# Optimization experiments

Hardware: AMD Instinct MI355X
Metric: run time of the kernel (lower is better)

Reference implementation:

```python
import jax, jax.numpy as jnp
import numpy as np


def _conv(x, w, b=None, stride=1, pad=1, groups=1):
    y = jax.lax.conv_general_dilated(
        x, w, (stride, stride), [(pad, pad), (pad, pad)],
        dimension_numbers=('NCHW', 'OIHW', 'NCHW'), feature_group_count=groups)
    return y if b is None else y + b[None, :, None, None]


def _dwt(x):
    # Haar DWT as grouped stride-2 conv, filters pre-flipped as in the torch code
    ll = np.array([[0.5, 0.5], [0.5, 0.5]])
    lh = np.array([[-0.5, -0.5], [0.5, 0.5]])
    hl = np.array([[-0.5, 0.5], [-0.5, 0.5]])
    hh = np.array([[0.5, -0.5], [-0.5, 0.5]])
    filts = np.stack([f[None, ::-1, ::-1] for f in (ll, lh, hl, hh)], 0)  # [4,1,2,2]
    w = jnp.asarray(np.concatenate([filts] * 3, 0), x.dtype)  # [12,1,2,2], groups=3
    return _conv(x, w, None, stride=2, pad=0, groups=3)


def setup_inputs():
    key = jax.random.key(0)
    ks = iter(jax.random.split(key, 64))
    def w(*shape):
        return jax.random.normal(next(ks), shape, jnp.float32) * 0.05
    B, H, W = 4, 512, 512
    F = 32  # number_f
    d = {'x': jax.random.uniform(next(ks), (B, 3, H, W), jnp.float32)}
    d['enc1_w'] = w(F, 3, 3, 3); d['enc1_b'] = w(F)
    for i in range(2, 6):
        d['enc%d_w' % i] = w(F, F, 3, 3); d['enc%d_b' % i] = w(F)
    d['cdc_w'] = w(F, F, 3, 3)                      # central-difference conv, no bias
    d['ct_w'] = w(64, 9, 3, 3); d['ct_b'] = w(64)   # conv_theta on 9-ch high_freq
    d['t1_w'] = w(64, 64, 1, 1); d['t1_b'] = w(64)
    d['t2_w'] = w(64, 64, 1, 1); d['t2_b'] = w(64)
    d['t3_w'] = w(1, 64, 1, 1); d['t3_b'] = w(1)
    d['lf_w'] = w(64, 3, 3, 3); d['lf_b'] = w(64)   # low_freq conv on haar_A
    d['fc1_w'] = w(512, 64); d['fc1_b'] = w(512)
    d['fc2_w'] = w(512, 512); d['fc2_b'] = w(512)
    d['fc3_w'] = w(512, 512); d['fc3_b'] = w(512)
    d['g_w'] = w(F, 512); d['g_b'] = w(F)           # to_gamma_0
    d['be_w'] = w(F, 512); d['be_b'] = w(F)         # to_beta_0
    d['res_w'] = w(F, F, 3, 3); d['res_b'] = w(F)
    d['d1_w'] = w(F, F, 3, 3); d['d1_b'] = w(F)
    d['d2_w'] = w(1, F, 3, 3); d['d2_b'] = w(1)
    return d


def reference(x, enc1_w, enc1_b, enc2_w, enc2_b, enc3_w, enc3_b, enc4_w, enc4_b,
              enc5_w, enc5_b, cdc_w, ct_w, ct_b, t1_w, t1_b, t2_w, t2_b, t3_w, t3_b,
              lf_w, lf_b, fc1_w, fc1_b, fc2_w, fc2_b, fc3_w, fc3_b,
              g_w, g_b, be_w, be_b, res_w, res_b, d1_w, d1_b, d2_w, d2_b):
    relu = jax.nn.relu
    # encoder
    f = relu(_conv(x, enc1_w, enc1_b))
    f = relu(_conv(f, enc2_w, enc2_b))
    f = relu(_conv(f, enc3_w, enc3_b))
    f = relu(_conv(f, enc4_w, enc4_b))
    f_org4 = relu(_conv(f, enc5_w, enc5_b))  # [B,32,H,W]
    # Haar wavelet split: per input channel blocks of 4 = (A,H,V,D)
    dwt = _dwt(x)                             # [B,12,H/2,W/2]
    haar_A = dwt[:, 0::4]                     # c1,c5,c9
    high_freq = jnp.concatenate([dwt[:, 1::4], dwt[:, 2::4], dwt[:, 3::4]], 1)  # [B,9,...]
    # theta net (Conv2d_cd)
    a = relu(_conv(high_freq, ct_w, ct_b))
    a = a.mean((2, 3), keepdims=True)         # adaptive avg pool to 1x1
    a = relu(_conv(a, t1_w, t1_b, pad=0))
    a = relu(_conv(a, t2_w, t2_b, pad=0))
    theta = jax.nn.sigmoid(_conv(a, t3_w, t3_b, pad=0))   # [B,1,1,1]
    out_normal = _conv(f_org4, cdc_w, None)
    kdiff = cdc_w.sum((2, 3))[:, :, None, None]            # [32,32,1,1]
    out_diff = _conv(f_org4, kdiff, None, pad=0)
    f_deco = relu(out_normal - theta * out_diff)           # [B,32,H,W]
    # attention / FiLM branch
    am = relu(_conv(haar_A, lf_w, lf_b)).mean((2, 3))      # [B,64]
    am = relu(am @ fc1_w.T + fc1_b)
    am = relu(am @ fc2_w.T + fc2_b)
    am = jax.nn.sigmoid(am @ fc3_w.T + fc3_b)              # [B,512]
    gamma = jax.nn.sigmoid(am @ g_w.T + g_b)[:, :, None, None]  # [B,32,1,1]
    beta = jnp.tanh(am @ be_w.T + be_b)[:, :, None, None]
    f = f_deco + gamma * _conv(f_deco, res_w, res_b) + beta
    # decoder
    f = relu(_conv(f, d1_w, d1_b))
    out_map = jnp.tanh(_conv(f, d2_w, d2_b))               # [B,1,H,W]
    enhance_image = x + out_map * (x * x - x)
    return enhance_image, out_map
```

## Files before the change

kernel.cpp:

```cpp
#include <hip/hip_runtime.h>
#include <hip/hip_bf16.h>
#include <cmath>

#define TPB 256

typedef __attribute__((ext_vector_type(8))) short s16x8;
typedef __attribute__((ext_vector_type(4))) float f32x4;
typedef unsigned short ushortT;

constexpr long long PSTR = 8454272;
constexpr int HW = 512 * 512;

static __device__ __forceinline__ short f2bf(float f) {
    union { __hip_bfloat16 h; short s; } u;
    u.h = __float2bfloat16(f);
    return u.s;
}
static __device__ __forceinline__ float bf2f(unsigned short u) {
    union { unsigned int i; float f; } v;
    v.i = ((unsigned int)u) << 16;
    return v.f;
}
static __device__ __forceinline__ unsigned int pack2(float a, float b) {
    return (unsigned int)(unsigned short)f2bf(a) | ((unsigned int)(unsigned short)f2bf(b) << 16);
}

#define GLOAD_LDS16(gp, lp) \
    __builtin_amdgcn_global_load_lds((const __attribute__((address_space(1))) void*)(gp), \
                                     (__attribute__((address_space(3))) void*)(lp), 16, 0, 0)

static __device__ void pack_body(const float* w, const float* bias, const float* theta,
                                 short* dst, int CO, int CI_src, int ci_off, int cog, int l)
{
    const int l15 = l & 15, sl = l >> 4;
    for (int t = 0; t < 9; ++t) {
        for (int mt = 0; mt < 2; ++mt) {
            const int co = cog * 32 + 16 * mt + l15;
            s16x8 p;
            #pragma unroll
            for (int i = 0; i < 8; ++i) {
                const int pci = 8 * sl + i;
                float val = 0.f;
                if (co < CO && pci >= ci_off && pci < ci_off + CI_src) {
                    const int ci = pci - ci_off;
                    val = w[((size_t)co * CI_src + ci) * 9 + t];
                    if (theta && t == 4) {
                        float s = 0.f;
                        for (int tt = 0; tt < 9; ++tt) s += w[((size_t)co * CI_src + ci) * 9 + tt];
                        val -= theta[0] * s;
                    }
                }
                p[i] = f2bf(val);
            }
            *(s16x8*)(dst + ((size_t)(t * 2 + mt) * 64 + l) * 8) = p;
        }
    }
    if (l < 32) {
        const int co = cog * 32 + l;
        ((float*)(dst + 9216))[l] = (bias && co < CO) ? bias[co] : 0.f;
    }
}

__global__ __launch_bounds__(64) void packall_k(
    const float* e1w, const float* e1b, const float* e2w, const float* e2b,
    const float* e3w, const float* e3b, const float* e4w, const float* e4b,
    const float* e5w, const float* e5b, const float* resw, const float* resb,
    const float* d1w, const float* d1b, const float* d2w, const float* d2b,
    const float* ctw, const float* ctb, const float* lfw, const float* lfb,
    short* wpack)
{
    const int s = blockIdx.x;
    const float *w, *b;
    int CO = 32, CI = 32, coff = 0, cog = 0;
    switch (s) {
        case 0: w = e1w; b = e1b; CI = 3; break;
        case 1: w = e2w; b = e2b; break;
        case 2: w = e3w; b = e3b; break;
        case 3: w = e4w; b = e4b; break;
        case 4: w = e5w; b = e5b; break;
        case 5: w = resw; b = resb; break;
        case 6: w = d1w; b = d1b; break;
        case 7: w = d2w; b = d2b; CO = 1; break;
        case 8: case 9: w = ctw; b = ctb; CO = 64; CI = 9; cog = s - 8; break;
        default: w = lfw; b = lfb; CO = 64; CI = 3; coff = 9; cog = s - 10; break;
    }
    pack_body(w, b, nullptr, wpack + (size_t)s * 10240, CO, CI, coff, cog, threadIdx.x);
}

__global__ __launch_bounds__(64) void packcdc_k(
    const float* cdcw, const float* theta, short* wpack)
{
    const int b = blockIdx.x;
    pack_body(cdcw, nullptr, theta + b, wpack + (size_t)(12 + b) * 10240, 32, 32, 0, 0, threadIdx.x);
}

__global__ __launch_bounds__(TPB) void zero_k(unsigned int* A2u, unsigned int* B2u)
{
    const int idx = blockIdx.x * TPB + threadIdx.x;
    if (idx >= 8 * 32832) return;
    const int q = idx / 32832, r = idx % 32832;
    unsigned int* P = (q < 4 ? A2u : B2u) + (size_t)(q & 3) * 4227136;
    const int RSU = 514 * 16;
    int off;
    if (r < 8224)       off = r;
    else if (r < 16448) off = 513 * RSU + (r - 8224);
    else if (r < 24640) { int u = r - 16448; off = (1 + (u >> 4)) * RSU + (u & 15); }
    else                { int u = r - 24640; off = (1 + (u >> 4)) * RSU + 513 * 16 + (u & 15); }
    P[off] = 0u;
}

__global__ __launch_bounds__(TPB) void ctlf_k(
    const float* __restrict__ x0p, const short* __restrict__ wpack8,
    float* __restrict__ part)
{
    constexpr int RSX = 66;
    constexpr int ROWB = RSX * 64;
    __shared__ s16x8 lds_t[6 * RSX * 4];
    __shared__ float s_red[4][32];
    char* sb = (char*)lds_t;

    const int z = blockIdx.z, cog = blockIdx.y;
    const int bid = blockIdx.x;
    const int x0 = (bid & 3) * 64, y0 = (bid >> 2) * 4;
    const int tid = threadIdx.x, lane = tid & 63, wv = tid >> 6;
    const int l15 = lane & 15, slot = lane >> 4;

    const short* wslot = wpack8 + (size_t)cog * 10240;
    const float* xz = x0p + (size_t)z * 3 * HW;

    s16x8 wf[9][2];
    #pragma unroll
    for (int t = 0; t < 9; ++t)
        #pragma unroll
        for (int mt = 0; mt < 2; ++mt)
            wf[t][mt] = *(const s16x8*)(wslot + ((size_t)(t * 2 + mt) * 64 + lane) * 8);

    #pragma unroll
    for (int j = 0; j < 2; ++j) {
        const int p = j * 256 + tid;
        if (p < 396) {
            const int row = p / 66, lx = p - row * 66;
            const int vs = (lx + (lx >> 2)) & 3;
            char* base = sb + (row * RSX + lx) * 64;
            const int sy = y0 + row - 1, sx = x0 + lx - 1;
            s16x8 pk0, pk1, zz;
            #pragma unroll
            for (int i = 0; i < 8; ++i) { pk0[i] = 0; pk1[i] = 0; zz[i] = 0; }
            if (sy >= 0 && sy < 256 && sx >= 0 && sx < 256) {
                #pragma unroll
                for (int c = 0; c < 3; ++c) {
                    const float* xp = xz + ((size_t)c * 512 + 2 * sy) * 512 + 2 * sx;
                    const float2 tp = *(const float2*)xp;
                    const float2 bt = *(const float2*)(xp + 512);
                    const float a = tp.x, b = tp.y, cc = bt.x, d = bt.y;
                    pk0[c]     = f2bf(0.5f * (a + b - cc - d));
                    pk0[3 + c] = f2bf(0.5f * (a - b + cc - d));
                    const float hh = 0.5f * (a - b - cc + d);
                    const float ll = 0.5f * (a + b + cc + d);
                    if (c < 2) pk0[6 + c] = f2bf(hh);
                    else       pk1[0]     = f2bf(hh);
                    pk1[1 + c] = f2bf(ll);
                }
            }
            *(s16x8*)(base + ((0 ^ vs) << 4)) = pk0;
            *(s16x8*)(base + ((1 ^ vs) << 4)) = pk1;
            *(s16x8*)(base + ((2 ^ vs) << 4)) = zz;
            *(s16x8*)(base + ((3 ^ vs) << 4)) = zz;
        }
    }
    __syncthreads();

    const int xw = 16 * wv;
    int roff[3];
    #pragma unroll
    for (int dx = 0; dx < 3; ++dx) {
        const int lx = xw + dx + l15;
        const int vs = (lx + (lx >> 2)) & 3;
        roff[dx] = lx * 64 + ((slot ^ vs) << 4);
    }
    const float* bptr = (const float*)(wslot + 9216);

    float ps[2][4];
    #pragma unroll
    for (int mt = 0; mt < 2; ++mt)
        #pragma unroll
        for (int reg = 0; reg < 4; ++reg) ps[mt][reg] = 0.f;

    #pragma unroll
    for (int r2 = 0; r2 < 4; r2 += 2) {
        f32x4 acc[2][2];
        #pragma unroll
        for (int a = 0; a < 2; ++a)
            #pragma unroll
            for (int b = 0; b < 2; ++b)
                #pragma unroll
                for (int e = 0; e < 4; ++e) acc[a][b][e] = 0.f;

        #pragma unroll
        for (int dy = 0; dy < 3; ++dy) {
            const int rb0 = (r2 + dy) * ROWB;
            #pragma unroll
            for (int dx = 0; dx < 3; ++dx) {
                const int tap = dy * 3 + dx;
                const s16x8 b0 = *(const s16x8*)(sb + rb0 + roff[dx]);
                const s16x8 b1 = *(const s16x8*)(sb + rb0 + ROWB + roff[dx]);
                #pragma unroll
                for (int mt = 0; mt < 2; ++mt) {
                    acc[0][mt] = __builtin_amdgcn_mfma_f32_16x16x32_bf16(wf[tap][mt], b0, acc[0][mt], 0, 0, 0);
                    acc[1][mt] = __builtin_amdgcn_mfma_f32_16x16x32_bf16(wf[tap][mt], b1, acc[1][mt], 0, 0, 0);
                }
            }
        }

        #pragma unroll
        for (int rr = 0; rr < 2; ++rr)
            #pragma unroll
            for (int mt = 0; mt < 2; ++mt)
                #pragma unroll
                for (int reg = 0; reg < 4; ++reg)
                    ps[mt][reg] += fmaxf(acc[rr][mt][reg] + bptr[16 * mt + 4 * slot + reg], 0.f);
    }

    #pragma unroll
    for (int mt = 0; mt < 2; ++mt)
        #pragma unroll
        for (int reg = 0; reg < 4; ++reg) {
            #pragma unroll
            for (int o = 1; o < 16; o <<= 1)
                ps[mt][reg] += __shfl_xor(ps[mt][reg], o, 64);
        }
    #pragma unroll
    for (int mt = 0; mt < 2; ++mt)
        #pragma unroll
        for (int reg = 0; reg < 4; ++reg)
            if (l15 == mt * 4 + reg)
                s_red[wv][16 * mt + 4 * slot + reg] = ps[mt][reg];
    __syncthreads();
    if (tid < 32) {
        const float s = s_red[0][tid] + s_red[1][tid] + s_red[2][tid] + s_red[3][tid];
        part[(((size_t)z * 4 + cog) * 256 + bid) * 32 + tid] = s;
    }
}

__global__ __launch_bounds__(TPB) void enc1n_k(
    const float* __restrict__ x0p, const short* __restrict__ wslot,
    ushortT* __restrict__ outP0)
{
    constexpr int RSX = 66;
    constexpr int ROWB = RSX * 64;
    __shared__ s16x8 lds_t[6 * RSX * 4];
    char* sb = (char*)lds_t;

    const int z = blockIdx.z;
    const float* xin = x0p + (size_t)z * 3 * HW;

    const int tid = threadIdx.x, lane = tid & 63, wv = tid >> 6;
    const int bid = blockIdx.x;
    const int swz = (bid & 7) * 128 + (bid >> 3);
    const int x0 = (swz & 7) * 64, y0 = (swz >> 3) * 4;
    const int l15 = lane & 15, slot = lane >> 4;

    s16x8 wf[9][2];
    #pragma unroll
    for (int t = 0; t < 9; ++t)
        #pragma unroll
        for (int mt = 0; mt < 2; ++mt)
            wf[t][mt] = *(const s16x8*)(wslot + ((size_t)(t * 2 + mt) * 64 + lane) * 8);

    #pragma unroll
    for (int j = 0; j < 2; ++j) {
        const int p = j * 256 + tid;
        if (p < 396) {
            const int row = p / 66, lx = p - row * 66;
            const int vs = (lx + (lx >> 2)) & 3;
            char* base = sb + (row * RSX + lx) * 64;
            const int gy = y0 + row - 1, gx = x0 + lx - 1;
            s16x8 pk, zz;
            #pragma unroll
            for (int i = 0; i < 8; ++i) { pk[i] = 0; zz[i] = 0; }
            if (gy >= 0 && gy < 512 && gx >= 0 && gx < 512) {
                #pragma unroll
                for (int c = 0; c < 3; ++c)
                    pk[c] = f2bf(xin[((size_t)c * 512 + gy) * 512 + gx]);
            }
            *(s16x8*)(base + ((0 ^ vs) << 4)) = pk;
            *(s16x8*)(base + ((1 ^ vs) << 4)) = zz;
            *(s16x8*)(base + ((2 ^ vs) << 4)) = zz;
            *(s16x8*)(base + ((3 ^ vs) << 4)) = zz;
        }
    }
    __syncthreads();

    const int xw = 16 * wv;
    int roff[3];
    #pragma unroll
    for (int dx = 0; dx < 3; ++dx) {
        const int lx = xw + dx + l15;
        const int vs = (lx + (lx >> 2)) & 3;
        roff[dx] = lx * 64 + ((slot ^ vs) << 4);
    }
    const float* bptr = (const float*)(wslot + 9216);
    ushortT* outP = outP0 + (size_t)z * PSTR;

    #pragma unroll
    for (int r2 = 0; r2 < 4; r2 += 2) {
        f32x4 acc[2][2];
        #pragma unroll
        for (int a = 0; a < 2; ++a)
            #pragma unroll
            for (int b = 0; b < 2; ++b)
                #pragma unroll
                for (int e = 0; e < 4; ++e) acc[a][b][e] = 0.f;

        #pragma unroll
        for (int dy = 0; dy < 3; ++dy) {
            const int rb0 = (r2 + dy) * ROWB;
            #pragma unroll
            for (int dx = 0; dx < 3; ++dx) {
                const int tap = dy * 3 + dx;
                const s16x8 b0 = *(const s16x8*)(sb + rb0 + roff[dx]);
                const s16x8 b1 = *(const s16x8*)(sb + rb0 + ROWB + roff[dx]);
                #pragma unroll
                for (int mt = 0; mt < 2; ++mt) {
                    acc[0][mt] = __builtin_amdgcn_mfma_f32_16x16x32_bf16(wf[tap][mt], b0, acc[0][mt], 0, 0, 0);
                    acc[1][mt] = __builtin_amdgcn_mfma_f32_16x16x32_bf16(wf[tap][mt], b1, acc[1][mt], 0, 0, 0);
                }
            }
        }

        #pragma unroll
        for (int rr = 0; rr < 2; ++rr) {
            const int gy = y0 + r2 + rr;
            const int gx = x0 + xw + l15;
            #pragma unroll
            for (int mt = 0; mt < 2; ++mt) {
                const size_t off = ((size_t)(gy + 1) * 514 + gx + 1) * 32 + 16 * mt + 4 * slot;
                float v[4];
                #pragma unroll
                for (int reg = 0; reg < 4; ++reg)
                    v[reg] = fmaxf(acc[rr][mt][reg] + bptr[16 * mt + 4 * slot + reg], 0.f);
                *(uint2*)(outP + off) = make_uint2(pack2(v[0], v[1]), pack2(v[2], v[3]));
            }
        }
    }
}

template<int EPI>
__global__ __launch_bounds__(TPB) void dconv64p_k(
    const ushortT* __restrict__ inP0, const short* __restrict__ wbase, int wstr,
    ushortT* __restrict__ outP0,
    const float* __restrict__ gamma0, const float* __restrict__ beta0,
    const float* __restrict__ xorig0, float* __restrict__ outE0, float* __restrict__ outM0)
{
    constexpr int MT = (EPI == 3) ? 1 : 2;
    constexpr int RSX = 66;
    constexpr int ROWB = RSX * 64;
    constexpr int BUFB = 6 * RSX * 64;
    __shared__ s16x8 lds_t[2 * 6 * RSX * 4];
    char* sbase = (char*)lds_t;

    const int z = blockIdx.z;
    const ushortT* inP = inP0 + (size_t)z * PSTR;
    const short* wslot = wbase + (size_t)z * wstr;

    const int tid = threadIdx.x, lane = tid & 63, wv = tid >> 6;
    const int bid = blockIdx.x;
    const int xcd = bid & 7, idx = bid >> 3;
    const int x0 = (idx & 7) * 64;
    const int yband = xcd * 2 + (idx >> 3);
    const int l15 = lane & 15, slot = lane >> 4;

    s16x8 wf[9][MT];
    #pragma unroll
    for (int t = 0; t < 9; ++t)
        #pragma unroll
        for (int mt = 0; mt < MT; ++mt)
            wf[t][mt] = *(const s16x8*)(wslot + ((size_t)(t * 2 + mt) * 64 + lane) * 8);

    const int xw = 16 * wv;
    int roff[3];
    #pragma unroll
    for (int dx = 0; dx < 3; ++dx) {
        const int lx = xw + dx + l15;
        const int vs = (lx + (lx >> 2)) & 3;
        roff[dx] = lx * 64 + ((slot ^ vs) << 4);
    }
    const float* bptr = (const float*)(wslot + 9216);

    auto stage = [&](int t, int b) {
        const int y0 = yband * 32 + 4 * t;
        char* sb = sbase + b * BUFB;
        #pragma unroll
        for (int j = 0; j < 6; ++j) {
            const int p = j * 256 + tid;
            const int row = p / 264;
            const int rem = p - row * 264;
            const int lx = rem >> 2, osl = rem & 3;
            const int o = osl ^ ((lx + (lx >> 2)) & 3);
            const ushortT* gp = inP + ((size_t)(y0 + row) * 514 + x0 + lx) * 32 + o * 8;
            GLOAD_LDS16(gp, sb + (size_t)(j * 256 + wv * 64) * 16);
        }
        if (tid < 48) {
            const int p = 1536 + tid;
            const int row = p / 264;
            const int rem = p - row * 264;
            const int lx = rem >> 2, osl = rem & 3;
            const int o = osl ^ ((lx + (lx >> 2)) & 3);
            const ushortT* gp = inP + ((size_t)(y0 + row) * 514 + x0 + lx) * 32 + o * 8;
            GLOAD_LDS16(gp, sb + (size_t)1536 * 16);
        }
    };

    stage(0, 0);

    #pragma unroll 1
    for (int t = 0; t < 8; ++t) {
        __syncthreads();
        if (t < 7) stage(t + 1, (t + 1) & 1);
        char* sb = sbase + (t & 1) * BUFB;
        const int y0t = yband * 32 + 4 * t;

        #pragma unroll
        for (int r2 = 0; r2 < 4; r2 += 2) {
            f32x4 acc[2][MT];
            #pragma unroll
            for (int a = 0; a < 2; ++a)
                #pragma unroll
                for (int b = 0; b < MT; ++b)
                    #pragma unroll
                    for (int e = 0; e < 4; ++e) acc[a][b][e] = 0.f;

            #pragma unroll
            for (int dy = 0; dy < 3; ++dy) {
                const int rb0 = (r2 + dy) * ROWB;
                #pragma unroll
                for (int dx = 0; dx < 3; ++dx) {
                    const int tap = dy * 3 + dx;
                    const s16x8 b0 = *(const s16x8*)(sb + rb0 + roff[dx]);
                    const s16x8 b1 = *(const s16x8*)(sb + rb0 + ROWB + roff[dx]);
                    #pragma unroll
                    for (int mt = 0; mt < MT; ++mt) {
                        acc[0][mt] = __builtin_amdgcn_mfma_f32_16x16x32_bf16(wf[tap][mt], b0, acc[0][mt], 0, 0, 0);
                        acc[1][mt] = __builtin_amdgcn_mfma_f32_16x16x32_bf16(wf[tap][mt], b1, acc[1][mt], 0, 0, 0);
                    }
                }
            }

            #pragma unroll
            for (int rr = 0; rr < 2; ++rr) {
                const int gy = y0t + r2 + rr;
                const int gx = x0 + xw + l15;
                if constexpr (EPI == 3) {
                    if (slot == 0) {
                        const float* xorig = xorig0 + (size_t)z * 3 * HW;
                        float* outE = outE0 + (size_t)z * 3 * HW;
                        float* outM = outM0 + (size_t)z * HW;
                        const float om = tanhf(acc[rr][0][0] + bptr[0]);
                        outM[(size_t)gy * 512 + gx] = om;
                        #pragma unroll
                        for (int c = 0; c < 3; ++c) {
                            const size_t xi = ((size_t)c * 512 + gy) * 512 + gx;
                            const float xv = xorig[xi];
                            outE[xi] = xv + om * (xv * xv - xv);
                        }
                    }
                } else {
                    ushortT* outP = outP0 + (size_t)z * PSTR;
                    #pragma unroll
                    for (int mt = 0; mt < MT; ++mt) {
                        const size_t off = ((size_t)(gy + 1) * 514 + gx + 1) * 32 + 16 * mt + 4 * slot;
                        float v[4];
                        #pragma unroll
                        for (int reg = 0; reg < 4; ++reg)
                            v[reg] = acc[rr][mt][reg] + bptr[16 * mt + 4 * slot + reg];
                        if constexpr (EPI == 0) {
                            #pragma unroll
                            for (int reg = 0; reg < 4; ++reg) v[reg] = fmaxf(v[reg], 0.f);
                        } else if constexpr (EPI == 2) {
                            const int prow = r2 + rr + 1;
                            const int lxr = xw + l15 + 1;
                            const int vsr = (lxr + (lxr >> 2)) & 3;
                            const int oo = (2 * mt + (slot >> 1)) ^ vsr;
                            const uint2 din = *(const uint2*)(sb + (prow * RSX + lxr) * 64 + (oo << 4) + ((slot & 1) << 3));
                            const float* gamma = gamma0 + 32 * z;
                            const float* beta  = beta0 + 32 * z;
                            const int cb = 16 * mt + 4 * slot;
                            v[0] = bf2f((unsigned short)(din.x & 0xffff)) + gamma[cb + 0] * v[0] + beta[cb + 0];
                            v[1] = bf2f((unsigned short)(din.x >> 16))    + gamma[cb + 1] * v[1] + beta[cb + 1];
                            v[2] = bf2f((unsigned short)(din.y & 0xffff)) + gamma[cb + 2] * v[2] + beta[cb + 2];
                            v[3] = bf2f((unsigned short)(din.y >> 16))    + gamma[cb + 3] * v[3] + beta[cb + 3];
                        }
                        *(uint2*)(outP + off) = make_uint2(pack2(v[0], v[1]), pack2(v[2], v[3]));
                    }
                }
            }
        }
    }
}

__global__ __launch_bounds__(TPB) void meanfin_k(
    const float* __restrict__ part, float* __restrict__ amean, float* __restrict__ am0)
{
    const int br = blockIdx.x;
    const int o = threadIdx.x;
    const int z = o >> 6, co = o & 63;
    const int cog = (br ? 2 : 0) + (co >> 5), c = co & 31;
    const float* p = part + (((size_t)z * 4 + cog) * 256) * 32 + c;
    float s = 0.f;
    for (int j = 0; j < 256; ++j) s += p[j * 32];
    (br ? am0 : amean)[z * 64 + co] = s * (1.f / 65536.f);
}

__global__ __launch_bounds__(64) void tchain_k(
    const float* __restrict__ amean,
    const float* __restrict__ t1w, const float* __restrict__ t1b,
    const float* __restrict__ t2w, const float* __restrict__ t2b,
    const float* __restrict__ t3w, const float* __restrict__ t3b,
    float* __restrict__ theta)
{
    const int b = blockIdx.x;
    const float* am = amean + b * 64;
    __shared__ float a0[64], a1[64], a2[64];
    const int co = threadIdx.x;
    a0[co] = am[co];
    __syncthreads();
    float s = t1b[co];
    #pragma unroll 8
    for (int ci = 0; ci < 64; ++ci) s = fmaf(t1w[co * 64 + ci], a0[ci], s);
    a1[co] = fmaxf(s, 0.f);
    __syncthreads();
    s = t2b[co];
    #pragma unroll 8
    for (int ci = 0; ci < 64; ++ci) s = fmaf(t2w[co * 64 + ci], a1[ci], s);
    a2[co] = fmaxf(s, 0.f);
    __syncthreads();
    if (co == 0) {
        float v = t3b[0];
        for (int ci = 0; ci < 64; ++ci) v = fmaf(t3w[ci], a2[ci], v);
        theta[b] = 1.f / (1.f + expf(-v));
    }
}

template<int ACT>
__global__ __launch_bounds__(TPB) void fcw_k(
    const float* __restrict__ in, const float* __restrict__ w,
    const float* __restrict__ bias, float* __restrict__ out, int K, int N)
{
    const int lane = threadIdx.x & 63, wv = threadIdx.x >> 6;
    const int idx = blockIdx.x * 4 + wv;
    if (idx >= 4 * N) return;
    const int b = idx / N, co = idx % N;
    float s = 0.f;
    for (int k = lane * 4; k < K; k += 256) {
        const float4 wv4 = *(const float4*)(w + (size_t)co * K + k);
        const float4 iv  = *(const float4*)(in + (size_t)b * K + k);
        s += wv4.x * iv.x + wv4.y * iv.y + wv4.z * iv.z + wv4.w * iv.w;
    }
    #pragma unroll
    for (int o = 32; o > 0; o >>= 1) s += __shfl_xor(s, o, 64);
    if (lane == 0) {
        s += bias[co];
        if (ACT == 0) s = fmaxf(s, 0.f);
        else if (ACT == 1) s = 1.f / (1.f + expf(-s));
        else s = tanhf(s);
        out[(size_t)b * N + co] = s;
    }
}

extern "C" void kernel_launch(void* const* d_in, const int* in_sizes, int n_in,
                              void* d_out, int out_size, void* d_ws, size_t ws_size,
                              hipStream_t stream)
{
    const float* x      = (const float*)d_in[0];
    const float* cdc_w  = (const float*)d_in[11];
    const float* t1_w   = (const float*)d_in[14];
    const float* t1_b   = (const float*)d_in[15];
    const float* t2_w   = (const float*)d_in[16];
    const float* t2_b   = (const float*)d_in[17];
    const float* t3_w   = (const float*)d_in[18];
    const float* t3_b   = (const float*)d_in[19];
    const float* fc1_w  = (const float*)d_in[22];
    const float* fc1_b  = (const float*)d_in[23];
    const float* fc2_w  = (const float*)d_in[24];
    const float* fc2_b  = (const float*)d_in[25];
    const float* fc3_w  = (const float*)d_in[26];
    const float* fc3_b  = (const float*)d_in[27];
    const float* g_w    = (const float*)d_in[28];
    const float* g_b    = (const float*)d_in[29];
    const float* be_w   = (const float*)d_in[30];
    const float* be_b   = (const float*)d_in[31];

    float* out = (float*)d_out;

    ushortT* A2 = (ushortT*)d_ws;
    ushortT* B2 = A2 + 4 * PSTR;
    float* part  = (float*)(B2 + 4 * PSTR);
    float* amean = part + 131072;
    float* am0   = amean + 256;
    float* am1   = am0 + 256;
    float* am2   = am1 + 2048;
    float* am3   = am2 + 2048;
    float* theta = am3 + 2048;
    float* gamma = theta + 4;
    float* beta  = gamma + 128;
    short* wpack = (short*)(beta + 128);
    const size_t need_bytes = (size_t)((char*)(wpack + 16 * 10240) - (char*)d_ws);
    if (ws_size < need_bytes) return;

    const dim3 blk(TPB);

    packall_k<<<dim3(12), dim3(64), 0, stream>>>(
        (const float*)d_in[1], (const float*)d_in[2], (const float*)d_in[3], (const float*)d_in[4],
        (const float*)d_in[5], (const float*)d_in[6], (const float*)d_in[7], (const float*)d_in[8],
        (const float*)d_in[9], (const float*)d_in[10], (const float*)d_in[32], (const float*)d_in[33],
        (const float*)d_in[34], (const float*)d_in[35], (const float*)d_in[36], (const float*)d_in[37],
        (const float*)d_in[12], (const float*)d_in[13], (const float*)d_in[20], (const float*)d_in[21],
        wpack);

    zero_k<<<dim3((8 * 32832 + TPB - 1) / TPB), blk, 0, stream>>>((unsigned int*)A2, (unsigned int*)B2);

    ctlf_k<<<dim3(256, 4, 4), blk, 0, stream>>>(x, wpack + 8 * 10240, part);

    meanfin_k<<<dim3(2), blk, 0, stream>>>(part, amean, am0);
    tchain_k<<<dim3(4), dim3(64), 0, stream>>>(amean, t1_w, t1_b, t2_w, t2_b, t3_w, t3_b, theta);
    fcw_k<0><<<dim3(512), blk, 0, stream>>>(am0, fc1_w, fc1_b, am1, 64, 512);
    fcw_k<0><<<dim3(512), blk, 0, stream>>>(am1, fc2_w, fc2_b, am2, 512, 512);
    fcw_k<1><<<dim3(512), blk, 0, stream>>>(am2, fc3_w, fc3_b, am3, 512, 512);
    fcw_k<1><<<dim3(32), blk, 0, stream>>>(am3, g_w, g_b, gamma, 512, 32);
    fcw_k<2><<<dim3(32), blk, 0, stream>>>(am3, be_w, be_b, beta, 512, 32);
    packcdc_k<<<dim3(4), dim3(64), 0, stream>>>(cdc_w, theta, wpack);

    const dim3 gE(1024, 1, 4);
    const dim3 gP(128, 1, 4);
    float* outM = out + (size_t)4 * 3 * HW;

    enc1n_k<<<gE, blk, 0, stream>>>(x, wpack, A2);
    dconv64p_k<0><<<gP, blk, 0, stream>>>(A2, wpack + 1 * 10240, 0, B2, nullptr, nullptr, nullptr, nullptr, nullptr);
    dconv64p_k<0><<<gP, blk, 0, stream>>>(B2, wpack + 2 * 10240, 0, A2, nullptr, nullptr, nullptr, nullptr, nullptr);
    dconv64p_k<0><<<gP, blk, 0, stream>>>(A2, wpack + 3 * 10240, 0, B2, nullptr, nullptr, nullptr, nullptr, nullptr);
    dconv64p_k<0><<<gP, blk, 0, stream>>>(B2, wpack + 4 * 10240, 0, A2, nullptr, nullptr, nullptr, nullptr, nullptr);
    dconv64p_k<0><<<gP, blk, 0, stream>>>(A2, wpack + 12 * 10240, 10240, B2, nullptr, nullptr, nullptr, nullptr, nullptr);
    dconv64p_k<2><<<gP, blk, 0, stream>>>(B2, wpack + 5 * 10240, 0, A2, gamma, beta, nullptr, nullptr, nullptr);
    dconv64p_k<0><<<gP, blk, 0, stream>>>(A2, wpack + 6 * 10240, 0, B2, nullptr, nullptr, nullptr, nullptr, nullptr);
    dconv64p_k<3><<<gP, blk, 0, stream>>>(B2, wpack + 7 * 10240, 0, nullptr, nullptr, nullptr, x, out, outM);
}
```

Before: 326.4 us.

## Fuse mean, theta chain, FC/FiLM MLP and cdc packing into one kernel

Replaces eight small launches (mean finalize, theta MLP, five FC layers, cdc weight packing) with a single kernel that runs one 256-thread block per batch item and keeps the intermediates in shared memory. The aim is to remove launch overhead and the global round-trips for the small intermediate vectors. In exchange, the FC layers now run on only four blocks. Each thread computes whole 512-long dot products with per-thread strided weight reads, so the 512x512 layers may become latency-bound and serialized.

```diff
diff --git a/kernel.cpp b/kernel.cpp
--- a/kernel.cpp
+++ b/kernel.cpp
@@ -87,13 +87,6 @@
     pack_body(w, b, nullptr, wpack + (size_t)s * 10240, CO, CI, coff, cog, threadIdx.x);
 }
 
-__global__ __launch_bounds__(64) void packcdc_k(
-    const float* cdcw, const float* theta, short* wpack)
-{
-    const int b = blockIdx.x;
-    pack_body(cdcw, nullptr, theta + b, wpack + (size_t)(12 + b) * 10240, 32, 32, 0, 0, threadIdx.x);
-}
-
 __global__ __launch_bounds__(TPB) void zero_k(unsigned int* A2u, unsigned int* B2u)
 {
     const int idx = blockIdx.x * TPB + threadIdx.x;
@@ -239,6 +232,80 @@
     if (tid < 32) {
         const float s = s_red[0][tid] + s_red[1][tid] + s_red[2][tid] + s_red[3][tid];
         part[(((size_t)z * 4 + cog) * 256 + bid) * 32 + tid] = s;
+    }
+}
+
+__global__ __launch_bounds__(TPB) void chainz_k(
+    const float* __restrict__ part,
+    const float* t1w, const float* t1b, const float* t2w, const float* t2b,
+    const float* t3w, const float* t3b,
+    const float* fc1w, const float* fc1b, const float* fc2w, const float* fc2b,
+    const float* fc3w, const float* fc3b,
+    const float* gw, const float* gbias, const float* bw, const float* bbias,
+    const float* cdcw,
+    float* __restrict__ gamma, float* __restrict__ beta, short* __restrict__ wpackcdc)
+{
+    const int z = blockIdx.x, tid = threadIdx.x;
+    __shared__ float amean[64], am0s[64], a1[64], a2[64];
+    __shared__ float am1[512], am2[512], am3[512];
+    __shared__ float th;
+
+    if (tid < 128) {
+        const int br = tid >> 6, co = tid & 63;
+        const int cog = (br ? 2 : 0) + (co >> 5), c = co & 31;
+        const float* p = part + (((size_t)z * 4 + cog) * 256) * 32 + c;
+        float s = 0.f;
+        for (int j = 0; j < 256; ++j) s += p[j * 32];
+        (br ? am0s : amean)[co] = s * (1.f / 65536.f);
+    }
+    __syncthreads();
+
+    if (tid < 64) {
+        float s = t1b[tid];
+        for (int ci = 0; ci < 64; ++ci) s = fmaf(t1w[tid * 64 + ci], amean[ci], s);
+        a1[tid] = fmaxf(s, 0.f);
+    }
+    for (int o = tid; o < 512; o += TPB) {
+        float s = fc1b[o];
+        for (int ci = 0; ci < 64; ++ci) s = fmaf(fc1w[(size_t)o * 64 + ci], am0s[ci], s);
+        am1[o] = fmaxf(s, 0.f);
+    }
+    __syncthreads();
+
+    if (tid < 64) {
+        float s = t2b[tid];
+        for (int ci = 0; ci < 64; ++ci) s = fmaf(t2w[tid * 64 + ci], a1[ci], s);
+        a2[tid] = fmaxf(s, 0.f);
+    }
+    for (int o = tid; o < 512; o += TPB) {
+        float s = fc2b[o];
+        for (int ci = 0; ci < 512; ++ci) s = fmaf(fc2w[(size_t)o * 512 + ci], am1[ci], s);
+        am2[o] = fmaxf(s, 0.f);
+    }
+    __syncthreads();
+
+    if (tid == 0) {
+        float v = t3b[0];
+        for (int ci = 0; ci < 64; ++ci) v = fmaf(t3w[ci], a2[ci], v);
+        th = 1.f / (1.f + expf(-v));
+    }
+    for (int o = tid; o < 512; o += TPB) {
+        float s = fc3b[o];
+        for (int ci = 0; ci < 512; ++ci) s = fmaf(fc3w[(size_t)o * 512 + ci], am2[ci], s);
+        am3[o] = 1.f / (1.f + expf(-s));
+    }
+    __syncthreads();
+
+    if (tid < 64) {
+        const int which = tid >> 5, co = tid & 31;
+        const float* w  = which ? bw : gw;
+        const float* bi = which ? bbias : gbias;
+        float s = bi[co];
+        for (int ci = 0; ci < 512; ++ci) s = fmaf(w[(size_t)co * 512 + ci], am3[ci], s);
+        if (which) beta[z * 32 + co] = tanhf(s);
+        else       gamma[z * 32 + co] = 1.f / (1.f + expf(-s));
+    } else if (tid < 128) {
+        pack_body(cdcw, nullptr, &th, wpackcdc + (size_t)z * 10240, 32, 32, 0, 0, tid - 64);
     }
 }
 
@@ -498,75 +565,6 @@
     }
 }
 
-__global__ __launch_bounds__(TPB) void meanfin_k(
-    const float* __restrict__ part, float* __restrict__ amean, float* __restrict__ am0)
-{
-    const int br = blockIdx.x;
-    const int o = threadIdx.x;
-    const int z = o >> 6, co = o & 63;
-    const int cog = (br ? 2 : 0) + (co >> 5), c = co & 31;
-    const float* p = part + (((size_t)z * 4 + cog) * 256) * 32 + c;
-    float s = 0.f;
-    for (int j = 0; j < 256; ++j) s += p[j * 32];
-    (br ? am0 : amean)[z * 64 + co] = s * (1.f / 65536.f);
-}
-
-__global__ __launch_bounds__(64) void tchain_k(
-    const float* __restrict__ amean,
-    const float* __restrict__ t1w, const float* __restrict__ t1b,
-    const float* __restrict__ t2w, const float* __restrict__ t2b,
-    const float* __restrict__ t3w, const float* __restrict__ t3b,
-    float* __restrict__ theta)
-{
-    const int b = blockIdx.x;
-    const float* am = amean + b * 64;
-    __shared__ float a0[64], a1[64], a2[64];
-    const int co = threadIdx.x;
-    a0[co] = am[co];
-    __syncthreads();
-    float s = t1b[co];
-    #pragma unroll 8
-    for (int ci = 0; ci < 64; ++ci) s = fmaf(t1w[co * 64 + ci], a0[ci], s);
-    a1[co] = fmaxf(s, 0.f);
-    __syncthreads();
-    s = t2b[co];
-    #pragma unroll 8
-    for (int ci = 0; ci < 64; ++ci) s = fmaf(t2w[co * 64 + ci], a1[ci], s);
-    a2[co] = fmaxf(s, 0.f);
-    __syncthreads();
-    if (co == 0) {
-        float v = t3b[0];
-        for (int ci = 0; ci < 64; ++ci) v = fmaf(t3w[ci], a2[ci], v);
-        theta[b] = 1.f / (1.f + expf(-v));
-    }
-}
-
-template<int ACT>
-__global__ __launch_bounds__(TPB) void fcw_k(
-    const float* __restrict__ in, const float* __restrict__ w,
-    const float* __restrict__ bias, float* __restrict__ out, int K, int N)
-{
-    const int lane = threadIdx.x & 63, wv = threadIdx.x >> 6;
-    const int idx = blockIdx.x * 4 + wv;
-    if (idx >= 4 * N) return;
-    const int b = idx / N, co = idx % N;
-    float s = 0.f;
-    for (int k = lane * 4; k < K; k += 256) {
-        const float4 wv4 = *(const float4*)(w + (size_t)co * K + k);
-        const float4 iv  = *(const float4*)(in + (size_t)b * K + k);
-        s += wv4.x * iv.x + wv4.y * iv.y + wv4.z * iv.z + wv4.w * iv.w;
-    }
-    #pragma unroll
-    for (int o = 32; o > 0; o >>= 1) s += __shfl_xor(s, o, 64);
-    if (lane == 0) {
-        s += bias[co];
-        if (ACT == 0) s = fmaxf(s, 0.f);
-        else if (ACT == 1) s = 1.f / (1.f + expf(-s));
-        else s = tanhf(s);
-        out[(size_t)b * N + co] = s;
-    }
-}
-
 extern "C" void kernel_launch(void* const* d_in, const int* in_sizes, int n_in,
                               void* d_out, int out_size, void* d_ws, size_t ws_size,
                               hipStream_t stream)
@@ -595,13 +593,7 @@
     ushortT* A2 = (ushortT*)d_ws;
     ushortT* B2 = A2 + 4 * PSTR;
     float* part  = (float*)(B2 + 4 * PSTR);
-    float* amean = part + 131072;
-    float* am0   = amean + 256;
-    float* am1   = am0 + 256;
-    float* am2   = am1 + 2048;
-    float* am3   = am2 + 2048;
-    float* theta = am3 + 2048;
-    float* gamma = theta + 4;
+    float* gamma = part + 131072;
     float* beta  = gamma + 128;
     short* wpack = (short*)(beta + 128);
     const size_t need_bytes = (size_t)((char*)(wpack + 16 * 10240) - (char*)d_ws);
@@ -621,14 +613,11 @@
 
     ctlf_k<<<dim3(256, 4, 4), blk, 0, stream>>>(x, wpack + 8 * 10240, part);
 
-    meanfin_k<<<dim3(2), blk, 0, stream>>>(part, amean, am0);
-    tchain_k<<<dim3(4), dim3(64), 0, stream>>>(amean, t1_w, t1_b, t2_w, t2_b, t3_w, t3_b, theta);
-    fcw_k<0><<<dim3(512), blk, 0, stream>>>(am0, fc1_w, fc1_b, am1, 64, 512);
-    fcw_k<0><<<dim3(512), blk, 0, stream>>>(am1, fc2_w, fc2_b, am2, 512, 512);
-    fcw_k<1><<<dim3(512), blk, 0, stream>>>(am2, fc3_w, fc3_b, am3, 512, 512);
-    fcw_k<1><<<dim3(32), blk, 0, stream>>>(am3, g_w, g_b, gamma, 512, 32);
-    fcw_k<2><<<dim3(32), blk, 0, stream>>>(am3, be_w, be_b, beta, 512, 32);
-    packcdc_k<<<dim3(4), dim3(64), 0, stream>>>(cdc_w, theta, wpack);
+    chainz_k<<<dim3(4), blk, 0, stream>>>(part,
+        t1_w, t1_b, t2_w, t2_b, t3_w, t3_b,
+        fc1_w, fc1_b, fc2_w, fc2_b, fc3_w, fc3_b,
+        g_w, g_b, be_w, be_b, cdc_w,
+        gamma, beta, wpack + 12 * 10240);
 
     const dim3 gE(1024, 1, 4);
     const dim3 gP(128, 1, 4);
```

Result: slower. 359.5 us (+10.1%).
